# Optimization experiments

Measured on AMD Instinct MI355X. Metric: run time of the kernel, lower is better.

The kernel has to match this reference:

```python
import jax, jax.numpy as jnp
import numpy as np

L1 = 512
LX = 32
COUNT = 8


def setup_inputs() -> dict:
    key = jax.random.key(0)
    ks = jax.random.split(key, 9)
    B = 65536
    x = jax.random.uniform(ks[0], (B, 2 * L1), dtype=jnp.float32)  # NNUE accumulator is in [0,1]
    ls_indices = jax.random.randint(ks[1], (B,), 0, COUNT, dtype=jnp.int64)
    # params (scaled ~1/sqrt(fan_in))
    w_fact = jax.random.normal(ks[2], (LX, 2 * L1), dtype=jnp.float32) * (1.0 / np.sqrt(2 * L1))
    w0 = jax.random.normal(ks[3], (LX * COUNT, 2 * L1), dtype=jnp.float32) * (1.0 / np.sqrt(2 * L1))
    b0 = jax.random.normal(ks[4], (LX * COUNT,), dtype=jnp.float32) * 0.05
    w1 = jax.random.normal(ks[5], (LX * COUNT, LX), dtype=jnp.float32) * (1.0 / np.sqrt(LX))
    b1 = jax.random.normal(ks[6], (LX * COUNT,), dtype=jnp.float32) * 0.05
    w2 = jax.random.normal(ks[7], (1 * COUNT, LX), dtype=jnp.float32) * (1.0 / np.sqrt(LX))
    b2 = jax.random.normal(ks[8], (1 * COUNT,), dtype=jnp.float32) * 0.05
    return {"x": x, "ls_indices": ls_indices, "w_fact": w_fact,
            "w0": w0, "b0": b0, "w1": w1, "b1": b1, "w2": w2, "b2": b2}


def _stack_linear_gather(h, w, b, idx, out_dim):
    # dense Linear for all COUNT buckets, then gather the selected bucket per row
    y = (h @ w.T + b).reshape(-1, COUNT, out_dim)          # [B, COUNT, out_dim]
    return y.reshape(-1, out_dim)[idx]                      # [B, out_dim]


def reference(x, ls_indices, w_fact, w0, b0, w1, b1, w2, b2):
    B = x.shape[0]
    idx = ls_indices.astype(jnp.int32) + jnp.arange(B, dtype=jnp.int32) * COUNT
    l1f = x @ w_fact.T                                      # [B, LX]
    h = _stack_linear_gather(x, w0, b0, idx, LX) + l1f      # layer 0 + factorized term
    h = jnp.clip(h, 0.0, 1.0)
    h = _stack_linear_gather(h, w1, b1, idx, LX)            # hidden layer 1
    h = jnp.clip(h, 0.0, 1.0)
    out = _stack_linear_gather(h, w2, b2, idx, 1)           # output layer (no clamp)
    return out
```

## Files before the change

kernel.cpp:

```cpp
#include <hip/hip_runtime.h>


#define B_ROWS 65536
#define LK     1024
#define TILE   32
#define NBLK   (B_ROWS / TILE)
#define KC     128
#define NCH    (LK / KC)
#define SROW   264
#define BUFSZ  (TILE * SROW)

#define BKT_OFF 524288

typedef short  short8  __attribute__((ext_vector_type(8)));
typedef float  f32x16  __attribute__((ext_vector_type(16)));

__device__ __forceinline__ unsigned pkbf(float a, float b) {
    unsigned ua = __float_as_uint(a), ub = __float_as_uint(b);
    ua = (ua + 0x7FFFu + ((ua >> 16) & 1u)) >> 16;
    ub = (ub + 0x7FFFu + ((ub >> 16) & 1u)) >> 16;
    return (ua & 0xFFFFu) | (ub << 16);
}

__device__ __forceinline__ unsigned cvtpk(float a, float b) {
    unsigned r;
    asm("v_cvt_pk_bf16_f32 %0, %1, %2" : "=v"(r) : "v"(a), "v"(b));
    return r;
}

__device__ __forceinline__ bool detect_i64(const int* p) {
    int acc = 0;
#pragma unroll
    for (int i = 0; i < 64; ++i) acc |= p[2 * i + 1];
    return acc == 0;
}

__device__ __forceinline__ int load_bucket(const int* p, int r, bool i64) {
    return (i64 ? p[2 * r] : p[r]) & 7;
}

__global__ __launch_bounds__(1024) void k_prep(
    const int* __restrict__ idx, const float* __restrict__ w0,
    const float* __restrict__ wf, uint4* __restrict__ wB,
    unsigned char* __restrict__ bktg)
{
    int t = threadIdx.x;
    if (blockIdx.x == 32) {
        __shared__ int s_i64;
        if (t == 0) s_i64 = detect_i64(idx) ? 1 : 0;
        __syncthreads();
        bool i64 = (s_i64 != 0);
#pragma unroll 4
        for (int j = 0; j < 64; ++j)
            bktg[j * 1024 + t] = (unsigned char)load_bucket(idx, j * 1024 + t, i64);
        return;
    }
    int f = blockIdx.x * 1024 + t;
    int b   = f >> 12;
    int i12 = f & 4095;
    int kc  = i12 >> 8;
    int i8  = i12 & 255;
    int n   = i8 & 31;
    int khi = i8 >> 5;
    int k = kc * 64 + khi * 8;
    const float* p0 = w0 + (size_t)(b * 32 + n) * LK + k;
    const float* pf = wf + (size_t)n * LK + k;
    float v[8];
#pragma unroll
    for (int j = 0; j < 8; ++j) v[j] = p0[j] + pf[j];
    uint4 o;
    o.x = pkbf(v[0], v[1]); o.y = pkbf(v[2], v[3]);
    o.z = pkbf(v[4], v[5]); o.w = pkbf(v[6], v[7]);
    wB[f] = o;
}

__global__ __launch_bounds__(256, 3) void k_main(
    const float* __restrict__ x, const unsigned char* __restrict__ bktg,
    const uint4* __restrict__ wB, const float* __restrict__ b0,
    const float* __restrict__ w1, const float* __restrict__ b1,
    const float* __restrict__ w2, const float* __restrict__ b2,
    float* __restrict__ out)
{
    __shared__ __align__(16) unsigned char a_s[2 * BUFSZ];
    __shared__ float hb[TILE * 36];
    __shared__ int   bkt_s[TILE];

    int row0 = blockIdx.x * TILE;
    int t    = threadIdx.x;
    int lane = t & 63;
    int wv   = t >> 6;
    int hi   = lane >> 5;
    int nn   = lane & 31;

    if (t < TILE) bkt_s[t] = (int)bktg[row0 + t];

    const float4* gp = (const float4*)x + (size_t)(row0 + (t >> 5)) * 256 + (t & 31);
    const int wb_off = (t >> 5) * SROW + (t & 31) * 8;

    float4 v[4];
#pragma unroll
    for (int q = 0; q < 4; ++q) v[q] = gp[q * 2048];
#pragma unroll
    for (int q = 0; q < 4; ++q) {
        uint2 o; o.x = cvtpk(v[q].x, v[q].y); o.y = cvtpk(v[q].z, v[q].w);
        *(uint2*)(a_s + wb_off + q * 8 * SROW) = o;
    }
    __syncthreads();

    const uint4* wB0 = wB + (size_t)(2 * wv) * 4096 + lane;
    const uint4* wB1 = wB0 + 4096;

    f32x16 acc0, acc1;
#pragma unroll
    for (int i = 0; i < 16; ++i) { acc0[i] = 0.0f; acc1[i] = 0.0f; }

    union UAB { uint4 u; short8 s8; };

    for (int ck = 0; ck < NCH; ++ck) {
        const unsigned char* cur = a_s + (ck & 1) * BUFSZ;
        unsigned char* nxt = a_s + ((ck + 1) & 1) * BUFSZ;

        UAB w0r[8], w1r[8];
#pragma unroll
        for (int cc = 0; cc < 8; ++cc) w0r[cc].u = wB0[(ck * 8 + cc) * 64];
#pragma unroll
        for (int cc = 0; cc < 8; ++cc) w1r[cc].u = wB1[(ck * 8 + cc) * 64];

        if (ck + 1 < NCH) {
#pragma unroll
            for (int q = 0; q < 4; ++q) v[q] = gp[q * 2048 + (ck + 1) * 32];
        }

        const unsigned char* Ab = cur + (size_t)(lane & 31) * SROW + 16 * hi;
#pragma unroll
        for (int cc = 0; cc < 8; ++cc) {
            UAB ua;
            ua.u = *(const uint4*)(Ab + 32 * cc);
            acc0 = __builtin_amdgcn_mfma_f32_32x32x16_bf16(ua.s8, w0r[cc].s8, acc0, 0, 0, 0);
            acc1 = __builtin_amdgcn_mfma_f32_32x32x16_bf16(ua.s8, w1r[cc].s8, acc1, 0, 0, 0);
        }

        if (ck + 1 < NCH) {
#pragma unroll
            for (int q = 0; q < 4; ++q) {
                uint2 o; o.x = cvtpk(v[q].x, v[q].y); o.y = cvtpk(v[q].z, v[q].w);
                *(uint2*)(nxt + wb_off + q * 8 * SROW) = o;
            }
        }
        __syncthreads();
    }

    int bb0 = 2 * wv, bb1 = 2 * wv + 1;
#pragma unroll
    for (int i = 0; i < 16; ++i) {
        int m = (i & 3) + 8 * (i >> 2) + 4 * hi;
        int mb = bkt_s[m];
        if (mb == bb0 || mb == bb1) {
            float s = (mb == bb0) ? acc0[i] : acc1[i];
            float h = s + b0[mb * 32 + nn];
            hb[m * 36 + nn] = fminf(fmaxf(h, 0.0f), 1.0f);
        }
    }
    __syncthreads();

    if (t < 64) {
        int r = t >> 1, half = t & 1;
        int bkt = bkt_s[r];
        const float4* hr = (const float4*)(hb + r * 36);
        float4 ha[8];
#pragma unroll
        for (int q = 0; q < 8; ++q) ha[q] = hr[q];
        const float* w1b = w1 + (size_t)bkt * 1024;
        const float* b1b = b1 + bkt * 32;
        const float* w2b = w2 + bkt * 32;
        float partial = 0.0f;
#pragma unroll
        for (int jj = 0; jj < 16; ++jj) {
            int j2 = half * 16 + jj;
            const float4* wr = (const float4*)&w1b[j2 * 32];
            float s = b1b[j2];
#pragma unroll
            for (int q = 0; q < 8; ++q) {
                float4 w4 = wr[q];
                s += ha[q].x * w4.x + ha[q].y * w4.y + ha[q].z * w4.z + ha[q].w * w4.w;
            }
            s = fminf(fmaxf(s, 0.0f), 1.0f);
            partial += s * w2b[j2];
        }
        partial += __shfl_xor(partial, 1);
        if (half == 0) out[row0 + r] = partial + b2[bkt];
    }
}

extern "C" void kernel_launch(void* const* d_in, const int* in_sizes, int n_in,
                              void* d_out, int out_size, void* d_ws, size_t ws_size,
                              hipStream_t stream) {
    const float* x   = (const float*)d_in[0];
    const int*   lsi = (const int*)  d_in[1];
    const float* wf  = (const float*)d_in[2];
    const float* w0  = (const float*)d_in[3];
    const float* b0  = (const float*)d_in[4];
    const float* w1  = (const float*)d_in[5];
    const float* b1  = (const float*)d_in[6];
    const float* w2  = (const float*)d_in[7];
    const float* b2  = (const float*)d_in[8];
    float* out = (float*)d_out;

    char* ws = (char*)d_ws;
    uint4* wB = (uint4*)ws;
    unsigned char* bktg = (unsigned char*)(ws + BKT_OFF);

    k_prep<<<33, 1024, 0, stream>>>(lsi, w0, wf, wB, bktg);
    k_main<<<NBLK, 256, 0, stream>>>(x, bktg, wB, b0, w1, b1, w2, b2, out);
}
```

Baseline: 417.8 us.

## Enlarge row tile to 128 and halve K chunk to reuse weights across row tiles

Each block now processes 128 rows instead of 32, issuing four 32-row MFMA sub-tiles per loaded weight fragment, so every weight load from global memory is reused four times. The K chunk is halved to 64 to keep the double-buffered LDS footprint bounded, and occupancy hint drops from 3 to 2 blocks per CU. The epilogue now uses all 256 threads for the 128 rows. This cuts redundant weight traffic but increases register pressure (eight accumulator tiles) and the number of per-chunk barriers.

```diff
diff --git a/kernel.cpp b/kernel.cpp
--- a/kernel.cpp
+++ b/kernel.cpp
@@ -3,11 +3,11 @@
 
 #define B_ROWS 65536
 #define LK     1024
-#define TILE   32
+#define TILE   128
 #define NBLK   (B_ROWS / TILE)
-#define KC     128
+#define KC     64
 #define NCH    (LK / KC)
-#define SROW   264
+#define SROW   136
 #define BUFSZ  (TILE * SROW)
 
 #define BKT_OFF 524288
@@ -74,7 +74,7 @@
     wB[f] = o;
 }
 
-__global__ __launch_bounds__(256, 3) void k_main(
+__global__ __launch_bounds__(256, 2) void k_main(
     const float* __restrict__ x, const unsigned char* __restrict__ bktg,
     const uint4* __restrict__ wB, const float* __restrict__ b0,
     const float* __restrict__ w1, const float* __restrict__ b1,
@@ -94,57 +94,65 @@
 
     if (t < TILE) bkt_s[t] = (int)bktg[row0 + t];
 
-    const float4* gp = (const float4*)x + (size_t)(row0 + (t >> 5)) * 256 + (t & 31);
-    const int wb_off = (t >> 5) * SROW + (t & 31) * 8;
-
-    float4 v[4];
-#pragma unroll
-    for (int q = 0; q < 4; ++q) v[q] = gp[q * 2048];
-#pragma unroll
-    for (int q = 0; q < 4; ++q) {
+    const float4* gp = (const float4*)x + (size_t)(row0 + (t >> 4)) * 256 + (t & 15);
+    const int wb_off = (t >> 4) * SROW + (t & 15) * 8;
+
+    float4 v[8];
+#pragma unroll
+    for (int q = 0; q < 8; ++q) v[q] = gp[q * 4096];
+#pragma unroll
+    for (int q = 0; q < 8; ++q) {
         uint2 o; o.x = cvtpk(v[q].x, v[q].y); o.y = cvtpk(v[q].z, v[q].w);
-        *(uint2*)(a_s + wb_off + q * 8 * SROW) = o;
+        *(uint2*)(a_s + wb_off + q * (16 * SROW)) = o;
     }
     __syncthreads();
 
     const uint4* wB0 = wB + (size_t)(2 * wv) * 4096 + lane;
     const uint4* wB1 = wB0 + 4096;
 
-    f32x16 acc0, acc1;
-#pragma unroll
-    for (int i = 0; i < 16; ++i) { acc0[i] = 0.0f; acc1[i] = 0.0f; }
+    f32x16 acc0[4], acc1[4];
+#pragma unroll
+    for (int rt = 0; rt < 4; ++rt)
+#pragma unroll
+        for (int i = 0; i < 16; ++i) { acc0[rt][i] = 0.0f; acc1[rt][i] = 0.0f; }
 
     union UAB { uint4 u; short8 s8; };
+    const int abase = (lane & 31) * SROW + 16 * hi;
 
     for (int ck = 0; ck < NCH; ++ck) {
         const unsigned char* cur = a_s + (ck & 1) * BUFSZ;
         unsigned char* nxt = a_s + ((ck + 1) & 1) * BUFSZ;
 
-        UAB w0r[8], w1r[8];
-#pragma unroll
-        for (int cc = 0; cc < 8; ++cc) w0r[cc].u = wB0[(ck * 8 + cc) * 64];
-#pragma unroll
-        for (int cc = 0; cc < 8; ++cc) w1r[cc].u = wB1[(ck * 8 + cc) * 64];
+        UAB w0r[4], w1r[4];
+#pragma unroll
+        for (int cc = 0; cc < 4; ++cc) w0r[cc].u = wB0[(ck * 4 + cc) * 64];
+#pragma unroll
+        for (int cc = 0; cc < 4; ++cc) w1r[cc].u = wB1[(ck * 4 + cc) * 64];
 
         if (ck + 1 < NCH) {
 #pragma unroll
-            for (int q = 0; q < 4; ++q) v[q] = gp[q * 2048 + (ck + 1) * 32];
-        }
-
-        const unsigned char* Ab = cur + (size_t)(lane & 31) * SROW + 16 * hi;
-#pragma unroll
-        for (int cc = 0; cc < 8; ++cc) {
-            UAB ua;
-            ua.u = *(const uint4*)(Ab + 32 * cc);
-            acc0 = __builtin_amdgcn_mfma_f32_32x32x16_bf16(ua.s8, w0r[cc].s8, acc0, 0, 0, 0);
-            acc1 = __builtin_amdgcn_mfma_f32_32x32x16_bf16(ua.s8, w1r[cc].s8, acc1, 0, 0, 0);
+            for (int q = 0; q < 8; ++q) v[q] = gp[q * 4096 + (ck + 1) * 16];
+        }
+
+#pragma unroll
+        for (int rt = 0; rt < 4; ++rt) {
+            const unsigned char* Ab = cur + rt * (32 * SROW) + abase;
+#pragma unroll
+            for (int cc = 0; cc < 4; ++cc) {
+                UAB ua;
+                ua.u = *(const uint4*)(Ab + 32 * cc);
+                acc0[rt] = __builtin_amdgcn_mfma_f32_32x32x16_bf16(
+                               ua.s8, w0r[cc].s8, acc0[rt], 0, 0, 0);
+                acc1[rt] = __builtin_amdgcn_mfma_f32_32x32x16_bf16(
+                               ua.s8, w1r[cc].s8, acc1[rt], 0, 0, 0);
+            }
         }
 
         if (ck + 1 < NCH) {
 #pragma unroll
-            for (int q = 0; q < 4; ++q) {
+            for (int q = 0; q < 8; ++q) {
                 uint2 o; o.x = cvtpk(v[q].x, v[q].y); o.y = cvtpk(v[q].z, v[q].w);
-                *(uint2*)(nxt + wb_off + q * 8 * SROW) = o;
+                *(uint2*)(nxt + wb_off + q * (16 * SROW)) = o;
             }
         }
         __syncthreads();
@@ -152,18 +160,21 @@
 
     int bb0 = 2 * wv, bb1 = 2 * wv + 1;
 #pragma unroll
-    for (int i = 0; i < 16; ++i) {
-        int m = (i & 3) + 8 * (i >> 2) + 4 * hi;
-        int mb = bkt_s[m];
-        if (mb == bb0 || mb == bb1) {
-            float s = (mb == bb0) ? acc0[i] : acc1[i];
-            float h = s + b0[mb * 32 + nn];
-            hb[m * 36 + nn] = fminf(fmaxf(h, 0.0f), 1.0f);
+    for (int rt = 0; rt < 4; ++rt) {
+#pragma unroll
+        for (int i = 0; i < 16; ++i) {
+            int m = rt * 32 + (i & 3) + 8 * (i >> 2) + 4 * hi;
+            int mb = bkt_s[m];
+            if (mb == bb0 || mb == bb1) {
+                float s = (mb == bb0) ? acc0[rt][i] : acc1[rt][i];
+                float h = s + b0[mb * 32 + nn];
+                hb[m * 36 + nn] = fminf(fmaxf(h, 0.0f), 1.0f);
+            }
         }
     }
     __syncthreads();
 
-    if (t < 64) {
+    {
         int r = t >> 1, half = t & 1;
         int bkt = bkt_s[r];
         const float4* hr = (const float4*)(hb + r * 36);
```

Result: slower. 446.1 us (+6.8%).
